# Performance work log

Hardware: AMD Instinct MI355X
Metric: run time of the kernel (lower is better)

Reference implementation:

```python
import jax, jax.numpy as jnp
import numpy as np

B, T, C, N = 4, 1024, 1024, 64
H = C // N
# dims = [max(32, 32*round(fac*C**p/32))] per module formula for C=1024
D_W, D_A, D_V, D_G = 64, 64, 32, 160
GN_EPS = 0.00064


def setup_inputs() -> dict:
    key = jax.random.key(0)
    keys = iter(jax.random.split(key, 40))

    def rn(shape, s=0.02):
        return jax.random.normal(next(keys), shape, jnp.float32) * s

    return {
        "x": jax.random.normal(next(keys), (B, T, C), jnp.float32),
        "v_first": jax.random.normal(next(keys), (B, T, C), jnp.float32),
        "x_r": rn((1, 1, C), 0.5), "x_w": rn((1, 1, C), 0.5), "x_k": rn((1, 1, C), 0.5),
        "x_v": rn((1, 1, C), 0.5), "x_a": rn((1, 1, C), 0.5), "x_g": rn((1, 1, C), 0.5),
        "w0": rn((1, 1, C), 0.5) - 1.0, "w1": rn((C, D_W)), "w2": rn((D_W, C)),
        "a0": rn((1, 1, C), 0.5), "a1": rn((C, D_A)), "a2": rn((D_A, C)),
        "v0p": rn((1, 1, C), 0.5), "v1": rn((C, D_V)), "v2": rn((D_V, C)),
        "g1": rn((C, D_G)), "g2": rn((D_G, C)),
        "k_k": rn((1, 1, C), 0.2) + 0.8, "k_a": rn((1, 1, C), 0.2) + 1.0,
        "r_k": rn((H, N), 0.5),
        "W_r": rn((C, C)), "W_k": rn((C, C)), "W_v": rn((C, C)), "W_o": rn((C, C)),
        "gn_w": jnp.ones((C,), jnp.float32), "gn_b": jnp.zeros((C,), jnp.float32),
    }


def _group_norm(x2, wgt, bias):
    # torch GroupNorm(H groups, C channels) on [B*T, C]: normalize each N-chunk
    xg = x2.reshape(x2.shape[0], H, N)
    mu = xg.mean(-1, keepdims=True)
    var = ((xg - mu) ** 2).mean(-1, keepdims=True)  # biased var, as torch
    xn = (xg - mu) * jax.lax.rsqrt(var + GN_EPS)
    return xn.reshape(x2.shape) * wgt + bias


def rwkv7_recurrence(r, w, k, v, a, b):
    # RWKV-7 chunked-cuda semantics (wind_rwkv naive reference), all [B,T,H,N];
    # w is the per-channel decay exp(-exp(w_raw)) in (0,1).
    # state s: [B,H,N,N], s[i,j] ~ value_i x key_j
    # s_t = s_{t-1} * diag(w_t) + (s_{t-1} @ a_t) outer b_t + v_t outer k_t
    # y_t = s_t @ r_t
    def step(s, inp):
        r_t, w_t, k_t, v_t, a_t, b_t = inp  # each [B,H,N]
        sa = jnp.einsum('bhij,bhj->bhi', s, a_t)
        s = (s * w_t[:, :, None, :]
             + sa[..., None] * b_t[:, :, None, :]
             + v_t[..., None] * k_t[:, :, None, :])
        y = jnp.einsum('bhij,bhj->bhi', s, r_t)
        return s, y

    xs = tuple(jnp.swapaxes(t, 0, 1) for t in (r, w, k, v, a, b))  # [T,B,H,N]
    s0 = jnp.zeros((r.shape[0], r.shape[2], r.shape[3], r.shape[3]), r.dtype)
    _, ys = jax.lax.scan(step, s0, xs)
    return jnp.swapaxes(ys, 0, 1)  # [B,T,H,N]


def reference(x, v_first, x_r, x_w, x_k, x_v, x_a, x_g, w0, w1, w2, a0, a1, a2,
              v0p, v1, v2, g1, g2, k_k, k_a, r_k, W_r, W_k, W_v, W_o, gn_w, gn_b):
    Bx, Tx, Cx = x.shape
    # F.pad(x, (0,0,1,-1)): shift tokens right by one, zero at t=0
    last_x = jnp.concatenate([jnp.zeros_like(x[:, :1]), x[:, :-1]], axis=1)
    dx = last_x - x
    xr, xw, xk, xv, xa, xg = (x + m * dx for m in (x_r, x_w, x_k, x_v, x_a, x_g))
    r = xr @ W_r.T
    w = -jax.nn.softplus(-w0 - jnp.tanh(xw @ w1) @ w2) - 0.5
    k = xk @ W_k.T
    v = xv @ W_v.T
    v = v + (v_first - v) * jax.nn.sigmoid(v0p + (xv @ v1) @ v2)
    a = jax.nn.sigmoid(a0 + (xa @ a1) @ a2)
    g = jax.nn.sigmoid(xg @ g1) @ g2
    kk = k * k_k
    k = k * (1.0 + (a - 1.0) * k_a)
    rs, ws, ks, vs, kks, aa = (t.reshape(Bx, Tx, H, N) for t in (r, w, k, v, kk, a))
    # F.normalize(kk, dim=-1) with eps clamp 1e-12
    kks = kks / jnp.maximum(jnp.linalg.norm(kks, axis=-1, keepdims=True), 1e-12)
    wdec = jnp.exp(-jnp.exp(ws))
    y = rwkv7_recurrence(rs, wdec, ks, vs, kks, -kks * aa)  # [B,T,H,N]
    yn = _group_norm(y.reshape(Bx * Tx, Cx), gn_w, gn_b).reshape(Bx, Tx, Cx)
    yn = yn + ((rs * ks * r_k).sum(-1, keepdims=True) * vs).reshape(Bx, Tx, Cx)
    return (yn * g) @ W_o.T
```

## Files before the change

kernel.cpp:

```cpp
#include <hip/hip_runtime.h>
#include <hip/hip_bf16.h>
#include <math.h>


using bf16 = __hip_bfloat16;
typedef __attribute__((ext_vector_type(8))) short bf16x8;
typedef __attribute__((ext_vector_type(4))) float f32x4;

#define DEVINL __device__ __forceinline__

DEVINL float b2f(bf16 v) { return __bfloat162float(v); }
DEVINL bf16 f2b(float f) { return __float2bfloat16(f); }
DEVINL float sigm(float x) { return 1.f / (1.f + __expf(-x)); }
DEVINL float bfbits2f(unsigned short s) { return __uint_as_float(((unsigned)s) << 16); }
DEVINL float ldin(const void* p, size_t i, int fl) {
  return fl ? ((const float*)p)[i] : b2f(((const bf16*)p)[i]);
}

DEVINL void g2lds16(const void* g, void* l) {
  __builtin_amdgcn_global_load_lds(
      (__attribute__((address_space(1))) void*)(g),
      (__attribute__((address_space(3))) void*)(l), 16, 0, 0);
}

template<int CTRL>
DEVINL float dpp_add(float x) {
  int t = __builtin_amdgcn_update_dpp(0, __float_as_int(x), CTRL, 0xf, 0xf, true);
  return x + __int_as_float(t);
}
DEVINL float rowsum16(float x) {
  x = dpp_add<0x121>(x);
  x = dpp_add<0x122>(x);
  x = dpp_add<0x124>(x);
  x = dpp_add<0x128>(x);
  return x;
}

__global__ void detect_kernel(const unsigned* __restrict__ x, int* __restrict__ flag) {
  __shared__ int cnt[4];
  int tid = threadIdx.x;
  unsigned w = x[tid];
  float v = fabsf(bfbits2f((unsigned short)(w & 0xffffu)));
  bool plaus = (v >= 1e-4f && v <= 16.f);
  unsigned long long m = __ballot(plaus);
  if ((tid & 63) == 0) cnt[tid >> 6] = __popcll(m);
  __syncthreads();
  if (tid == 0) *flag = (cnt[0] + cnt[1] + cnt[2] + cnt[3] < 128) ? 1 : 0;
}

__global__ __launch_bounds__(256)
void prep_kernel(const void* __restrict__ x,
    const void* mr, const void* mw, const void* mk,
    const void* mv, const void* ma, const void* mg,
    const void* W_r, const void* W_k, const void* W_v, const void* W_o,
    bf16* cWr, bf16* cWk, bf16* cWv, bf16* cWo,
    const void* w1, const void* w2, const void* a1, const void* a2,
    const void* v1, const void* v2, const void* g1, const void* g2,
    bf16* w1t, bf16* w2t, bf16* a1t, bf16* a2t,
    bf16* v1t, bf16* v2t, bf16* g1t, bf16* g2t,
    const int* __restrict__ flag,
    bf16* oxr, bf16* oxw, bf16* oxk, bf16* oxv, bf16* oxa, bf16* oxg)
{
  int fl = *flag;
  int bx = blockIdx.x;
  if (bx < 16384) {
    size_t idx = (size_t)bx * 256 + threadIdx.x;
    int c = (int)(idx & 1023);
    int t = (int)((idx >> 10) & 1023);
    float xc = ldin(x, idx, fl);
    float px = (t == 0) ? 0.f : ldin(x, idx - 1024, fl);
    float dx = px - xc;
    oxr[idx] = f2b(xc + ldin(mr, c, fl) * dx);
    oxw[idx] = f2b(xc + ldin(mw, c, fl) * dx);
    oxk[idx] = f2b(xc + ldin(mk, c, fl) * dx);
    oxv[idx] = f2b(xc + ldin(mv, c, fl) * dx);
    oxa[idx] = f2b(xc + ldin(ma, c, fl) * dx);
    oxg[idx] = f2b(xc + ldin(mg, c, fl) * dx);
  } else if (bx < 32768) {
    int g = (bx - 16384) * 256 + threadIdx.x;
    int seg = g >> 20, i = g & 1048575;
    const void* s = seg == 0 ? W_r : seg == 1 ? W_k : seg == 2 ? W_v : W_o;
    bf16* d = seg == 0 ? cWr : seg == 1 ? cWk : seg == 2 ? cWv : cWo;
    d[i] = fl ? f2b(((const float*)s)[i]) : ((const bf16*)s)[i];
  } else {
    int idx = (bx - 32768) * 256 + threadIdx.x;
    if (idx >= 655360) return;
    const int ends[8] = {65536, 131072, 196608, 262144, 294912, 327680, 491520, 655360};
    const int Ks[8] = {1024, 64, 1024, 64, 1024, 32, 1024, 160};
    const int Nd[8] = {64, 1024, 64, 1024, 32, 1024, 160, 1024};
    const void* srcs[8] = {w1, w2, a1, a2, v1, v2, g1, g2};
    bf16* dsts[8] = {w1t, w2t, a1t, a2t, v1t, v2t, g1t, g2t};
    int seg = 0, start = 0;
#pragma unroll
    for (int s2 = 0; s2 < 7; s2++)
      if (idx >= ends[s2]) { seg = s2 + 1; start = ends[s2]; }
    int local = idx - start;
    int K = Ks[seg], N = Nd[seg];
    int k = local / N, n = local - k * N;
    dsts[seg][(size_t)n * K + k] = f2b(ldin(srcs[seg], local, fl));
  }
}

template<typename Epi>
DEVINL void gemm_core(const bf16* __restrict__ A, const bf16* __restrict__ Bt,
                      int K, int Brows, int m0, int n0, Epi&& epi)
{
  __shared__ short As[128 * 32];
  __shared__ short Bs[128 * 32];
  const int tid = threadIdx.x;
  const int wid = tid >> 6, lane = tid & 63;
  const int wr = (wid >> 1) * 64, wc = (wid & 1) * 64;

  f32x4 acc[4][4] = {};

  const int lrow = lane >> 2;
  const int lcol = (lane & 3) * 8;
  int arow0 = m0 + (wid * 2 + 0) * 16 + lrow;
  int arow1 = m0 + (wid * 2 + 1) * 16 + lrow;
  int brow0 = n0 + (wid * 2 + 0) * 16 + lrow; if (brow0 >= Brows) brow0 = Brows - 1;
  int brow1 = n0 + (wid * 2 + 1) * 16 + lrow; if (brow1 >= Brows) brow1 = Brows - 1;

  const short* Ag = (const short*)A;
  const short* Bg = (const short*)Bt;

  for (int kk = 0; kk < K; kk += 32) {
    __syncthreads();
    g2lds16(Ag + (size_t)arow0 * K + kk + lcol, As + (wid * 2 + 0) * 512);
    g2lds16(Ag + (size_t)arow1 * K + kk + lcol, As + (wid * 2 + 1) * 512);
    g2lds16(Bg + (size_t)brow0 * K + kk + lcol, Bs + (wid * 2 + 0) * 512);
    g2lds16(Bg + (size_t)brow1 * K + kk + lcol, Bs + (wid * 2 + 1) * 512);
    __syncthreads();
    bf16x8 af[4], bfr[4];
#pragma unroll
    for (int mi = 0; mi < 4; mi++)
      af[mi] = *(const bf16x8*)(As + (wr + mi * 16 + (lane & 15)) * 32 + (lane >> 4) * 8);
#pragma unroll
    for (int ni = 0; ni < 4; ni++)
      bfr[ni] = *(const bf16x8*)(Bs + (wc + ni * 16 + (lane & 15)) * 32 + (lane >> 4) * 8);
#pragma unroll
    for (int mi = 0; mi < 4; mi++)
#pragma unroll
      for (int ni = 0; ni < 4; ni++)
        acc[mi][ni] = __builtin_amdgcn_mfma_f32_16x16x32_bf16(af[mi], bfr[ni], acc[mi][ni], 0, 0, 0);
  }

  const int cl0 = lane & 15, r0 = (lane >> 4) * 4;
#pragma unroll
  for (int mi = 0; mi < 4; mi++)
#pragma unroll
    for (int ni = 0; ni < 4; ni++) {
      int col = n0 + wc + ni * 16 + cl0;
#pragma unroll
      for (int rr = 0; rr < 4; rr++)
        epi(m0 + wr + mi * 16 + r0 + rr, col, acc[mi][ni][rr]);
    }
}

__global__ __launch_bounds__(256)
void stage1_kernel(const bf16* xw, const bf16* xa, const bf16* xv, const bf16* xg,
                   const bf16* w1t, const bf16* a1t, const bf16* v1t, const bf16* g1t,
                   bf16* hw, bf16* ha, bf16* hv, bf16* hg)
{
  int y = blockIdx.y;
  int seg = (y <= 2) ? y : 3;
  int n0 = (y == 4) ? 128 : 0;
  const bf16* A  = seg == 0 ? xw  : seg == 1 ? xa  : seg == 2 ? xv  : xg;
  const bf16* Bt = seg == 0 ? w1t : seg == 1 ? a1t : seg == 2 ? v1t : g1t;
  int NS         = seg == 0 ? 64  : seg == 1 ? 64  : seg == 2 ? 32  : 160;
  bf16* out      = seg == 0 ? hw  : seg == 1 ? ha  : seg == 2 ? hv  : hg;
  gemm_core(A, Bt, 1024, NS, blockIdx.x * 128, n0, [&](int row, int col, float f) {
    if (col >= NS) return;
    if (seg == 0) f = tanhf(f);
    else if (seg == 3) f = sigm(f);
    out[(size_t)row * NS + col] = f2b(f);
  });
}

__global__ __launch_bounds__(256)
void bigrkv_kernel(const bf16* xr, const bf16* xk, const bf16* xv,
                   const bf16* cWr, const bf16* cWk, const bf16* cWv,
                   bf16* __restrict__ PKb)
{
  int z = blockIdx.z;
  const bf16* A  = z == 0 ? xr  : z == 1 ? xk  : xv;
  const bf16* Bt = z == 0 ? cWr : z == 1 ? cWk : cWv;
  gemm_core(A, Bt, 1024, 1024, blockIdx.x * 128, blockIdx.y * 128,
            [&](int row, int col, float f) {
    PKb[(size_t)row * 5120 + (col >> 6) * 320 + z * 64 + (col & 63)] = f2b(f);
  });
}

__global__ __launch_bounds__(256)
void stage2_kernel(const bf16* hw, const bf16* ha, const bf16* hv, const bf16* hg,
                   const bf16* w2t, const bf16* a2t, const bf16* v2t, const bf16* g2t,
                   bf16* __restrict__ PKb, float* __restrict__ PKw, float* __restrict__ G,
                   const void* w0, const void* a0, const void* v0p, const void* vfirst,
                   const int* __restrict__ flag)
{
  int fl = *flag;
  int z = blockIdx.z;
  const bf16* A  = z == 0 ? hw  : z == 1 ? ha  : z == 2 ? hv  : hg;
  const bf16* Bt = z == 0 ? w2t : z == 1 ? a2t : z == 2 ? v2t : g2t;
  int K          = z == 0 ? 64  : z == 1 ? 64  : z == 2 ? 32  : 160;
  gemm_core(A, Bt, K, 1024, blockIdx.x * 128, blockIdx.y * 128,
            [&](int row, int col, float f) {
    if (z == 0) {
      float zz = -(ldin(w0, col, fl) + f);
      float sp = fmaxf(zz, 0.f) + __logf(1.f + __expf(-fabsf(zz)));
      PKw[(size_t)row * 1024 + col] = __expf(-__expf(-sp - 0.5f));
    } else if (z == 1) {
      PKb[(size_t)row * 5120 + (col >> 6) * 320 + 192 + (col & 63)] =
          f2b(sigm(ldin(a0, col, fl) + f));
    } else if (z == 2) {
      float sg = sigm(ldin(v0p, col, fl) + f);
      size_t pa = (size_t)row * 5120 + (col >> 6) * 320 + 128 + (col & 63);
      float vr = b2f(PKb[pa]);
      float vf = ldin(vfirst, (size_t)row * 1024 + col, fl);
      PKb[pa] = f2b(vr + (vf - vr) * sg);
    } else {
      G[(size_t)row * 1024 + col] = f;
    }
  });
}

__global__ __launch_bounds__(256)
void post_kernel(bf16* __restrict__ PKb, const void* __restrict__ kkw,
                 const void* __restrict__ kaw, const int* __restrict__ flag) {
  int fl = *flag;
  int slot = blockIdx.x * 4 + (threadIdx.x >> 6);
  int tg = slot >> 4, h = slot & 15;
  int n = threadIdx.x & 63, c = h * 64 + n;
  size_t pb = (size_t)tg * 5120 + (size_t)h * 320;
  float kraw = b2f(PKb[pb + 64 + n]);
  float asig = b2f(PKb[pb + 192 + n]);
  float kk = kraw * ldin(kkw, c, fl);
  float ss = kk * kk;
  ss += __shfl_xor(ss, 1);  ss += __shfl_xor(ss, 2);  ss += __shfl_xor(ss, 4);
  ss += __shfl_xor(ss, 8);  ss += __shfl_xor(ss, 16); ss += __shfl_xor(ss, 32);
  float kkn = kk / fmaxf(sqrtf(ss), 1e-12f);
  PKb[pb + 192 + n] = f2b(kkn);
  PKb[pb + 256 + n] = f2b(-kkn * asig);
  PKb[pb + 64 + n]  = f2b(kraw * (1.f + (asig - 1.f) * ldin(kaw, c, fl)));
}

#define RD 8
__global__ __launch_bounds__(64, 1)
void recur_kernel(const bf16* __restrict__ PKb, const float* __restrict__ PKw,
                  float* __restrict__ Y) {
  int blk = blockIdx.x;
  int bh = blk & 63, sib = blk >> 6;
  int b = bh >> 4, h = bh & 15;
  int lane = threadIdx.x;
  int jq = lane & 15, j0 = jq * 4;
  int rl = lane >> 4;
  int i = sib * 4 + rl;

  const unsigned short* pb =
      (const unsigned short*)(PKb) + ((size_t)b * 1024 * 16 + h) * 320;
  const float* pw = PKw + (size_t)b * 1024 * 1024 + h * 64;
  float* yout = Y + (size_t)b * 1024 * 1024 + h * 64 + i;

  uint2 Lr[RD], Lk[RD], La[RD], Lb[RD];
  float4 Lw[RD];
  unsigned short Lv[RD];

#pragma unroll
  for (int d = 0; d < RD; ++d) {
    const unsigned short* s = pb + (size_t)d * 5120;
    Lr[d] = *(const uint2*)(s + j0);
    Lk[d] = *(const uint2*)(s + 64 + j0);
    La[d] = *(const uint2*)(s + 192 + j0);
    Lb[d] = *(const uint2*)(s + 256 + j0);
    Lv[d] = s[128 + i];
    Lw[d] = *(const float4*)(pw + (size_t)d * 1024 + j0);
  }

  float S0 = 0.f, S1 = 0.f, S2 = 0.f, S3 = 0.f;

  for (int t0 = 0; t0 < 1024; t0 += RD) {
#pragma unroll
    for (int d = 0; d < RD; ++d) {
      int t = t0 + d;
      uint2 ur = Lr[d], uk = Lk[d], ua = La[d], ub = Lb[d];
      float4 wv = Lw[d];
      float vi = bfbits2f(Lv[d]);
      {
        const unsigned short* s = pb + (size_t)(t + RD) * 5120;
        Lr[d] = *(const uint2*)(s + j0);
        Lk[d] = *(const uint2*)(s + 64 + j0);
        La[d] = *(const uint2*)(s + 192 + j0);
        Lb[d] = *(const uint2*)(s + 256 + j0);
        Lv[d] = s[128 + i];
        Lw[d] = *(const float4*)(pw + (size_t)(t + RD) * 1024 + j0);
      }
      float ax = bfbits2f((unsigned short)(ua.x & 0xffffu)), ay = bfbits2f((unsigned short)(ua.x >> 16));
      float az = bfbits2f((unsigned short)(ua.y & 0xffffu)), aw = bfbits2f((unsigned short)(ua.y >> 16));
      float kx = bfbits2f((unsigned short)(uk.x & 0xffffu)), ky = bfbits2f((unsigned short)(uk.x >> 16));
      float kz = bfbits2f((unsigned short)(uk.y & 0xffffu)), kw = bfbits2f((unsigned short)(uk.y >> 16));
      float bx = bfbits2f((unsigned short)(ub.x & 0xffffu)), by = bfbits2f((unsigned short)(ub.x >> 16));
      float bz = bfbits2f((unsigned short)(ub.y & 0xffffu)), bw = bfbits2f((unsigned short)(ub.y >> 16));
      float rx = bfbits2f((unsigned short)(ur.x & 0xffffu)), ry = bfbits2f((unsigned short)(ur.x >> 16));
      float rz = bfbits2f((unsigned short)(ur.y & 0xffffu)), rw = bfbits2f((unsigned short)(ur.y >> 16));

      float sa = (S0 * ax + S1 * ay) + (S2 * az + S3 * aw);
      sa = rowsum16(sa);
      S0 = S0 * wv.x + (sa * bx + vi * kx);
      S1 = S1 * wv.y + (sa * by + vi * ky);
      S2 = S2 * wv.z + (sa * bz + vi * kz);
      S3 = S3 * wv.w + (sa * bw + vi * kw);
      float y = (S0 * rx + S1 * ry) + (S2 * rz + S3 * rw);
      y = rowsum16(y);
      if (jq == 0) yout[(size_t)t * 1024] = y;
    }
  }
}

__global__ __launch_bounds__(256)
void gn_kernel(const float* __restrict__ Y, const bf16* __restrict__ PKb,
               const float* __restrict__ G,
               const void* __restrict__ gw, const void* __restrict__ gb,
               const void* __restrict__ rk, const int* __restrict__ flag,
               bf16* __restrict__ Z)
{
  int fl = *flag;
  int slot = blockIdx.x * 4 + (threadIdx.x >> 6);
  int tg = slot >> 4, h = slot & 15;
  int n = threadIdx.x & 63, c = h * 64 + n;
  size_t pb = (size_t)tg * 5120 + (size_t)h * 320;
  float y = Y[(size_t)tg * 1024 + c];
  float rr = b2f(PKb[pb + n]), kf = b2f(PKb[pb + 64 + n]), vv = b2f(PKb[pb + 128 + n]);
  float s1 = y, s2 = y * y, s3 = rr * kf * ldin(rk, c, fl);
#pragma unroll
  for (int m = 1; m < 64; m <<= 1) {
    s1 += __shfl_xor(s1, m);
    s2 += __shfl_xor(s2, m);
    s3 += __shfl_xor(s3, m);
  }
  float mu = s1 * 0.015625f;
  float var = s2 * 0.015625f - mu * mu;
  float xn = (y - mu) * rsqrtf(var + 0.00064f);
  float yn = xn * ldin(gw, c, fl) + ldin(gb, c, fl);
  yn += s3 * vv;
  Z[(size_t)tg * 1024 + c] = f2b(yn * G[(size_t)tg * 1024 + c]);
}

__global__ __launch_bounds__(256)
void outgemm_kernel(const bf16* Z, const bf16* cWo,
                    float* oF, bf16* oB, const int* __restrict__ flag)
{
  int fl = *flag;
  gemm_core(Z, cWo, 1024, 1024, blockIdx.x * 128, blockIdx.y * 128,
            [&](int row, int col, float f) {
    if (fl) oF[(size_t)row * 1024 + col] = f;
    else    oB[(size_t)row * 1024 + col] = f2b(f);
  });
}

extern "C" void kernel_launch(void* const* d_in, const int* in_sizes, int n_in,
                              void* d_out, int out_size, void* d_ws, size_t ws_size,
                              hipStream_t stream)
{
  const void* x      = d_in[0];
  const void* vfirst = d_in[1];
  const void* m_r = d_in[2];  const void* m_w = d_in[3];
  const void* m_k = d_in[4];  const void* m_v = d_in[5];
  const void* m_a = d_in[6];  const void* m_g = d_in[7];
  const void* w0  = d_in[8];  const void* w1  = d_in[9];  const void* w2  = d_in[10];
  const void* a0  = d_in[11]; const void* a1  = d_in[12]; const void* a2  = d_in[13];
  const void* v0p = d_in[14]; const void* v1  = d_in[15]; const void* v2  = d_in[16];
  const void* g1  = d_in[17]; const void* g2  = d_in[18];
  const void* k_k = d_in[19]; const void* k_a = d_in[20]; const void* r_k = d_in[21];
  const void* W_r = d_in[22]; const void* W_k = d_in[23];
  const void* W_v = d_in[24]; const void* W_o = d_in[25];
  const void* gnw = d_in[26]; const void* gnb = d_in[27];
  (void)in_sizes; (void)n_in; (void)out_size; (void)ws_size;

  char* ws = (char*)d_ws;
  size_t off = 0;
  auto alloc = [&](size_t bytes) -> void* {
    void* p = ws + off; off += (bytes + 255) & ~(size_t)255; return p;
  };
  const size_t BTC2 = (size_t)4096 * 1024 * 2;
  int*  flag = (int*)alloc(256);
  bf16* cWr = (bf16*)alloc((size_t)1048576 * 2);
  bf16* cWk = (bf16*)alloc((size_t)1048576 * 2);
  bf16* cWv = (bf16*)alloc((size_t)1048576 * 2);
  bf16* cWo = (bf16*)alloc((size_t)1048576 * 2);
  bf16* w1t = (bf16*)alloc((size_t)65536 * 2);
  bf16* w2t = (bf16*)alloc((size_t)65536 * 2);
  bf16* a1t = (bf16*)alloc((size_t)65536 * 2);
  bf16* a2t = (bf16*)alloc((size_t)65536 * 2);
  bf16* v1t = (bf16*)alloc((size_t)32768 * 2);
  bf16* v2t = (bf16*)alloc((size_t)32768 * 2);
  bf16* g1t = (bf16*)alloc((size_t)163840 * 2);
  bf16* g2t = (bf16*)alloc((size_t)163840 * 2);
  bf16* xr = (bf16*)alloc(BTC2);
  bf16* xw = (bf16*)alloc(BTC2);
  bf16* xk = (bf16*)alloc(BTC2);
  bf16* xv = (bf16*)alloc(BTC2);
  bf16* xa = (bf16*)alloc(BTC2);
  bf16* xg = (bf16*)alloc(BTC2);
  bf16* PKb = (bf16*)alloc((size_t)4096 * 5120 * 2);
  float* PKw = (float*)alloc((size_t)4096 * 1024 * 4);
  bf16* hw  = (bf16*)alloc((size_t)4096 * 64 * 2);
  bf16* ha  = (bf16*)alloc((size_t)4096 * 64 * 2);
  bf16* hv  = (bf16*)alloc((size_t)4096 * 32 * 2);
  bf16* hg  = (bf16*)alloc((size_t)4096 * 160 * 2);
  float* G = (float*)xr;
  float* Y = (float*)xk;
  bf16*  Z = xa;

  detect_kernel<<<1, 256, 0, stream>>>((const unsigned*)x, flag);
  prep_kernel<<<35328, 256, 0, stream>>>(
      x, m_r, m_w, m_k, m_v, m_a, m_g,
      W_r, W_k, W_v, W_o, cWr, cWk, cWv, cWo,
      w1, w2, a1, a2, v1, v2, g1, g2,
      w1t, w2t, a1t, a2t, v1t, v2t, g1t, g2t,
      flag, xr, xw, xk, xv, xa, xg);

  stage1_kernel<<<dim3(32, 5), 256, 0, stream>>>(xw, xa, xv, xg,
                                                 w1t, a1t, v1t, g1t, hw, ha, hv, hg);
  bigrkv_kernel<<<dim3(32, 8, 3), 256, 0, stream>>>(xr, xk, xv, cWr, cWk, cWv, PKb);
  stage2_kernel<<<dim3(32, 8, 4), 256, 0, stream>>>(hw, ha, hv, hg,
                                                    w2t, a2t, v2t, g2t,
                                                    PKb, PKw, G, w0, a0, v0p, vfirst, flag);
  post_kernel<<<16384, 256, 0, stream>>>(PKb, k_k, k_a, flag);
  recur_kernel<<<1024, 64, 0, stream>>>(PKb, PKw, Y);
  gn_kernel<<<16384, 256, 0, stream>>>(Y, PKb, G, gnw, gnb, r_k, flag, Z);
  outgemm_kernel<<<dim3(32, 8), 256, 0, stream>>>(Z, cWo, (float*)d_out, (bf16*)d_out, flag);
}
```

Baseline: 574.5 us.

## Repack recurrence inputs into per-head contiguous stream, double-buffer via LDS

```diff
diff --git a/kernel.cpp b/kernel.cpp
--- a/kernel.cpp
+++ b/kernel.cpp
@@ -13,6 +13,8 @@
 DEVINL bf16 f2b(float f) { return __float2bfloat16(f); }
 DEVINL float sigm(float x) { return 1.f / (1.f + __expf(-x)); }
 DEVINL float bfbits2f(unsigned short s) { return __uint_as_float(((unsigned)s) << 16); }
+DEVINL float lo16(unsigned u) { return __uint_as_float(u << 16); }
+DEVINL float hi16(unsigned u) { return __uint_as_float(u & 0xffff0000u); }
 DEVINL float ldin(const void* p, size_t i, int fl) {
   return fl ? ((const float*)p)[i] : b2f(((const bf16*)p)[i]);
 }
@@ -21,6 +23,12 @@
   __builtin_amdgcn_global_load_lds(
       (__attribute__((address_space(1))) void*)(g),
       (__attribute__((address_space(3))) void*)(l), 16, 0, 0);
+}
+
+DEVINL void wait_vmcnt8() {
+  __asm__ volatile("" ::: "memory");
+  __builtin_amdgcn_s_waitcnt(0x0F78);
+  __asm__ volatile("" ::: "memory");
 }
 
 template<int CTRL>
@@ -34,6 +42,10 @@
   x = dpp_add<0x124>(x);
   x = dpp_add<0x128>(x);
   return x;
+}
+
+DEVINL size_t stream_sb(int row, int h) {
+  return ((size_t)((row >> 10) * 16 + h) * 1024 + (row & 1023)) * 512;
 }
 
 __global__ void detect_kernel(const unsigned* __restrict__ x, int* __restrict__ flag) {
@@ -179,21 +191,24 @@
 __global__ __launch_bounds__(256)
 void bigrkv_kernel(const bf16* xr, const bf16* xk, const bf16* xv,
                    const bf16* cWr, const bf16* cWk, const bf16* cWv,
-                   bf16* __restrict__ PKb)
+                   bf16* __restrict__ STR)
 {
   int z = blockIdx.z;
   const bf16* A  = z == 0 ? xr  : z == 1 ? xk  : xv;
   const bf16* Bt = z == 0 ? cWr : z == 1 ? cWk : cWv;
   gemm_core(A, Bt, 1024, 1024, blockIdx.x * 128, blockIdx.y * 128,
             [&](int row, int col, float f) {
-    PKb[(size_t)row * 5120 + (col >> 6) * 320 + z * 64 + (col & 63)] = f2b(f);
+    size_t sb = stream_sb(row, col >> 6);
+    int n = col & 63;
+    size_t off = (z == 2) ? (sb + 256 + n) : (sb + n * 4 + z);
+    STR[off] = f2b(f);
   });
 }
 
 __global__ __launch_bounds__(256)
 void stage2_kernel(const bf16* hw, const bf16* ha, const bf16* hv, const bf16* hg,
                    const bf16* w2t, const bf16* a2t, const bf16* v2t, const bf16* g2t,
-                   bf16* __restrict__ PKb, float* __restrict__ PKw, float* __restrict__ G,
+                   bf16* __restrict__ STR, float* __restrict__ STRf, float* __restrict__ G,
                    const void* w0, const void* a0, const void* v0p, const void* vfirst,
                    const int* __restrict__ flag)
 {
@@ -204,19 +219,19 @@
   int K          = z == 0 ? 64  : z == 1 ? 64  : z == 2 ? 32  : 160;
   gemm_core(A, Bt, K, 1024, blockIdx.x * 128, blockIdx.y * 128,
             [&](int row, int col, float f) {
+    int n = col & 63;
     if (z == 0) {
       float zz = -(ldin(w0, col, fl) + f);
       float sp = fmaxf(zz, 0.f) + __logf(1.f + __expf(-fabsf(zz)));
-      PKw[(size_t)row * 1024 + col] = __expf(-__expf(-sp - 0.5f));
+      STRf[stream_sb(row, col >> 6) / 2 + 160 + n] = __expf(-__expf(-sp - 0.5f));
     } else if (z == 1) {
-      PKb[(size_t)row * 5120 + (col >> 6) * 320 + 192 + (col & 63)] =
-          f2b(sigm(ldin(a0, col, fl) + f));
+      STR[stream_sb(row, col >> 6) + n * 4 + 2] = f2b(sigm(ldin(a0, col, fl) + f));
     } else if (z == 2) {
       float sg = sigm(ldin(v0p, col, fl) + f);
-      size_t pa = (size_t)row * 5120 + (col >> 6) * 320 + 128 + (col & 63);
-      float vr = b2f(PKb[pa]);
+      size_t pa = stream_sb(row, col >> 6) + 256 + n;
+      float vr = b2f(STR[pa]);
       float vf = ldin(vfirst, (size_t)row * 1024 + col, fl);
-      PKb[pa] = f2b(vr + (vf - vr) * sg);
+      STR[pa] = f2b(vr + (vf - vr) * sg);
     } else {
       G[(size_t)row * 1024 + col] = f;
     }
@@ -224,83 +239,69 @@
 }
 
 __global__ __launch_bounds__(256)
-void post_kernel(bf16* __restrict__ PKb, const void* __restrict__ kkw,
+void post_kernel(bf16* __restrict__ STR, const void* __restrict__ kkw,
                  const void* __restrict__ kaw, const int* __restrict__ flag) {
   int fl = *flag;
   int slot = blockIdx.x * 4 + (threadIdx.x >> 6);
   int tg = slot >> 4, h = slot & 15;
   int n = threadIdx.x & 63, c = h * 64 + n;
-  size_t pb = (size_t)tg * 5120 + (size_t)h * 320;
-  float kraw = b2f(PKb[pb + 64 + n]);
-  float asig = b2f(PKb[pb + 192 + n]);
+  size_t sb = stream_sb(tg, h);
+  float kraw = b2f(STR[sb + n * 4 + 1]);
+  float asig = b2f(STR[sb + n * 4 + 2]);
   float kk = kraw * ldin(kkw, c, fl);
   float ss = kk * kk;
   ss += __shfl_xor(ss, 1);  ss += __shfl_xor(ss, 2);  ss += __shfl_xor(ss, 4);
   ss += __shfl_xor(ss, 8);  ss += __shfl_xor(ss, 16); ss += __shfl_xor(ss, 32);
   float kkn = kk / fmaxf(sqrtf(ss), 1e-12f);
-  PKb[pb + 192 + n] = f2b(kkn);
-  PKb[pb + 256 + n] = f2b(-kkn * asig);
-  PKb[pb + 64 + n]  = f2b(kraw * (1.f + (asig - 1.f) * ldin(kaw, c, fl)));
-}
-
-#define RD 8
-__global__ __launch_bounds__(64, 1)
-void recur_kernel(const bf16* __restrict__ PKb, const float* __restrict__ PKw,
-                  float* __restrict__ Y) {
+  STR[sb + n * 4 + 2] = f2b(kkn);
+  STR[sb + n * 4 + 3] = f2b(-kkn * asig);
+  STR[sb + n * 4 + 1] = f2b(kraw * (1.f + (asig - 1.f) * ldin(kaw, c, fl)));
+}
+
+#define CH 8
+__global__ __launch_bounds__(64)
+void recur_kernel(const char* __restrict__ STR, float* __restrict__ Y) {
+  __shared__ __align__(16) char lds[2 * CH * 1024];
   int blk = blockIdx.x;
   int bh = blk & 63, sib = blk >> 6;
   int b = bh >> 4, h = bh & 15;
   int lane = threadIdx.x;
-  int jq = lane & 15, j0 = jq * 4;
-  int rl = lane >> 4;
+  int jq = lane & 15, rl = lane >> 4;
   int i = sib * 4 + rl;
 
-  const unsigned short* pb =
-      (const unsigned short*)(PKb) + ((size_t)b * 1024 * 16 + h) * 320;
-  const float* pw = PKw + (size_t)b * 1024 * 1024 + h * 64;
+  const char* gb = STR + (size_t)bh * (1024 * 1024) + lane * 16;
   float* yout = Y + (size_t)b * 1024 * 1024 + h * 64 + i;
 
-  uint2 Lr[RD], Lk[RD], La[RD], Lb[RD];
-  float4 Lw[RD];
-  unsigned short Lv[RD];
-
-#pragma unroll
-  for (int d = 0; d < RD; ++d) {
-    const unsigned short* s = pb + (size_t)d * 5120;
-    Lr[d] = *(const uint2*)(s + j0);
-    Lk[d] = *(const uint2*)(s + 64 + j0);
-    La[d] = *(const uint2*)(s + 192 + j0);
-    Lb[d] = *(const uint2*)(s + 256 + j0);
-    Lv[d] = s[128 + i];
-    Lw[d] = *(const float4*)(pw + (size_t)d * 1024 + j0);
-  }
+  const char* prk = lds + jq * 32;
+  const char* pv  = lds + 512 + i * 2;
+  const char* pw  = lds + 640 + jq * 16;
+
+#pragma unroll
+  for (int d = 0; d < CH; ++d)
+    g2lds16(gb + (size_t)d * 1024, lds + d * 1024);
 
   float S0 = 0.f, S1 = 0.f, S2 = 0.f, S3 = 0.f;
 
-  for (int t0 = 0; t0 < 1024; t0 += RD) {
-#pragma unroll
-    for (int d = 0; d < RD; ++d) {
-      int t = t0 + d;
-      uint2 ur = Lr[d], uk = Lk[d], ua = La[d], ub = Lb[d];
-      float4 wv = Lw[d];
-      float vi = bfbits2f(Lv[d]);
-      {
-        const unsigned short* s = pb + (size_t)(t + RD) * 5120;
-        Lr[d] = *(const uint2*)(s + j0);
-        Lk[d] = *(const uint2*)(s + 64 + j0);
-        La[d] = *(const uint2*)(s + 192 + j0);
-        Lb[d] = *(const uint2*)(s + 256 + j0);
-        Lv[d] = s[128 + i];
-        Lw[d] = *(const float4*)(pw + (size_t)(t + RD) * 1024 + j0);
-      }
-      float ax = bfbits2f((unsigned short)(ua.x & 0xffffu)), ay = bfbits2f((unsigned short)(ua.x >> 16));
-      float az = bfbits2f((unsigned short)(ua.y & 0xffffu)), aw = bfbits2f((unsigned short)(ua.y >> 16));
-      float kx = bfbits2f((unsigned short)(uk.x & 0xffffu)), ky = bfbits2f((unsigned short)(uk.x >> 16));
-      float kz = bfbits2f((unsigned short)(uk.y & 0xffffu)), kw = bfbits2f((unsigned short)(uk.y >> 16));
-      float bx = bfbits2f((unsigned short)(ub.x & 0xffffu)), by = bfbits2f((unsigned short)(ub.x >> 16));
-      float bz = bfbits2f((unsigned short)(ub.y & 0xffffu)), bw = bfbits2f((unsigned short)(ub.y >> 16));
-      float rx = bfbits2f((unsigned short)(ur.x & 0xffffu)), ry = bfbits2f((unsigned short)(ur.x >> 16));
-      float rz = bfbits2f((unsigned short)(ur.y & 0xffffu)), rw = bfbits2f((unsigned short)(ur.y >> 16));
+  for (int t0 = 0; t0 < 1024; t0 += CH) {
+    int cur = (t0 >> 3) & 1;
+    int cbase = cur * (CH * 1024);
+    char* bufn = lds + (cur ^ 1) * (CH * 1024);
+#pragma unroll
+    for (int d = 0; d < CH; ++d)
+      g2lds16(gb + (size_t)(t0 + CH + d) * 1024, bufn + d * 1024);
+    wait_vmcnt8();
+#pragma unroll
+    for (int d = 0; d < CH; ++d) {
+      int so = cbase + d * 1024;
+      uint4 m0 = *(const uint4*)(prk + so);
+      uint4 m1 = *(const uint4*)(prk + so + 16);
+      float4 wv = *(const float4*)(pw + so);
+      unsigned short vu = *(const unsigned short*)(pv + so);
+      float vi = bfbits2f(vu);
+      float rx = lo16(m0.x), kx = hi16(m0.x), ax = lo16(m0.y), bx = hi16(m0.y);
+      float ry = lo16(m0.z), ky = hi16(m0.z), ay = lo16(m0.w), by = hi16(m0.w);
+      float rz = lo16(m1.x), kz = hi16(m1.x), az = lo16(m1.y), bz = hi16(m1.y);
+      float rw = lo16(m1.z), kw = hi16(m1.z), aw = lo16(m1.w), bw = hi16(m1.w);
 
       float sa = (S0 * ax + S1 * ay) + (S2 * az + S3 * aw);
       sa = rowsum16(sa);
@@ -310,13 +311,13 @@
       S3 = S3 * wv.w + (sa * bw + vi * kw);
       float y = (S0 * rx + S1 * ry) + (S2 * rz + S3 * rw);
       y = rowsum16(y);
-      if (jq == 0) yout[(size_t)t * 1024] = y;
+      if (jq == 0) yout[(size_t)(t0 + d) * 1024] = y;
     }
   }
 }
 
 __global__ __launch_bounds__(256)
-void gn_kernel(const float* __restrict__ Y, const bf16* __restrict__ PKb,
+void gn_kernel(const float* __restrict__ Y, const bf16* __restrict__ STR,
                const float* __restrict__ G,
                const void* __restrict__ gw, const void* __restrict__ gb,
                const void* __restrict__ rk, const int* __restrict__ flag,
@@ -326,9 +327,9 @@
   int slot = blockIdx.x * 4 + (threadIdx.x >> 6);
   int tg = slot >> 4, h = slot & 15;
   int n = threadIdx.x & 63, c = h * 64 + n;
-  size_t pb = (size_t)tg * 5120 + (size_t)h * 320;
+  size_t sb = stream_sb(tg, h);
   float y = Y[(size_t)tg * 1024 + c];
-  float rr = b2f(PKb[pb + n]), kf = b2f(PKb[pb + 64 + n]), vv = b2f(PKb[pb + 128 + n]);
+  float rr = b2f(STR[sb + n * 4]), kf = b2f(STR[sb + n * 4 + 1]), vv = b2f(STR[sb + 256 + n]);
   float s1 = y, s2 = y * y, s3 = rr * kf * ldin(rk, c, fl);
 #pragma unroll
   for (int m = 1; m < 64; m <<= 1) {
@@ -400,8 +401,7 @@
   bf16* xv = (bf16*)alloc(BTC2);
   bf16* xa = (bf16*)alloc(BTC2);
   bf16* xg = (bf16*)alloc(BTC2);
-  bf16* PKb = (bf16*)alloc((size_t)4096 * 5120 * 2);
-  float* PKw = (float*)alloc((size_t)4096 * 1024 * 4);
+  char* STR = (char*)alloc((size_t)64 * 1024 * 1024 + 16384);
   bf16* hw  = (bf16*)alloc((size_t)4096 * 64 * 2);
   bf16* ha  = (bf16*)alloc((size_t)4096 * 64 * 2);
   bf16* hv  = (bf16*)alloc((size_t)4096 * 32 * 2);
@@ -420,12 +420,13 @@
 
   stage1_kernel<<<dim3(32, 5), 256, 0, stream>>>(xw, xa, xv, xg,
                                                  w1t, a1t, v1t, g1t, hw, ha, hv, hg);
-  bigrkv_kernel<<<dim3(32, 8, 3), 256, 0, stream>>>(xr, xk, xv, cWr, cWk, cWv, PKb);
+  bigrkv_kernel<<<dim3(32, 8, 3), 256, 0, stream>>>(xr, xk, xv, cWr, cWk, cWv, (bf16*)STR);
   stage2_kernel<<<dim3(32, 8, 4), 256, 0, stream>>>(hw, ha, hv, hg,
                                                     w2t, a2t, v2t, g2t,
-                                                    PKb, PKw, G, w0, a0, v0p, vfirst, flag);
-  post_kernel<<<16384, 256, 0, stream>>>(PKb, k_k, k_a, flag);
-  recur_kernel<<<1024, 64, 0, stream>>>(PKb, PKw, Y);
-  gn_kernel<<<16384, 256, 0, stream>>>(Y, PKb, G, gnw, gnb, r_k, flag, Z);
+                                                    (bf16*)STR, (float*)STR, G,
+                                                    w0, a0, v0p, vfirst, flag);
+  post_kernel<<<16384, 256, 0, stream>>>((bf16*)STR, k_k, k_a, flag);
+  recur_kernel<<<1024, 64, 0, stream>>>(STR, Y);
+  gn_kernel<<<16384, 256, 0, stream>>>(Y, (bf16*)STR, G, gnw, gnb, r_k, flag, Z);
   outgemm_kernel<<<dim3(32, 8), 256, 0, stream>>>(Z, cWo, (float*)d_out, (bf16*)d_out, flag);
 }
```

Measured after the change: 571.7 us. No clear change (-0.5%).
